# Optimization experiments

Measured on AMD Instinct MI355X. Metric: run time of the kernel, lower is better.

The kernel has to match this reference:

```python
import jax, jax.numpy as jnp
import numpy as np

N_NODES = 50000
N_EDGES = 800000
IN_F = 256
OUT_F = 64
HEADS = 4
NEG_SLOPE = 0.2


def setup_inputs() -> dict:
    key = jax.random.key(0)
    ks = jax.random.split(key, 6)
    x = jax.random.normal(ks[0], (N_NODES, IN_F), dtype=jnp.float32)
    edge_index = jax.random.randint(ks[1], (2, N_EDGES), 0, N_NODES, dtype=jnp.int32)
    edge_weight = jax.random.uniform(ks[2], (N_EDGES,), dtype=jnp.float32)
    # Xavier-uniform-ish scale for params
    gain = float(np.sqrt(2.0 / (1.0 + NEG_SLOPE ** 2)))
    w_bound = gain * np.sqrt(6.0 / (IN_F + OUT_F))
    a_bound = gain * np.sqrt(6.0 / (OUT_F + 1))
    W = jax.random.uniform(ks[3], (HEADS, IN_F, OUT_F), minval=-w_bound, maxval=w_bound, dtype=jnp.float32)
    a_src = jax.random.uniform(ks[4], (HEADS, OUT_F, 1), minval=-a_bound, maxval=a_bound, dtype=jnp.float32)
    a_dst = jax.random.uniform(ks[5], (HEADS, OUT_F, 1), minval=-a_bound, maxval=a_bound, dtype=jnp.float32)
    return {"x": x, "edge_index": edge_index, "edge_weight": edge_weight,
            "W": W, "a_src": a_src, "a_dst": a_dst}


def reference(x, edge_index, edge_weight, W, a_src, a_dst):
    num_nodes = x.shape[0]
    # Per-head linear projection: [H, N, out]
    h = jnp.einsum('ni,hio->hno', x, W)
    # Per-node attention logits, [H, N]
    attn_src = jnp.einsum('hno,hod->hn', h, a_src)
    attn_dst = jnp.einsum('hno,hod->hn', h, a_dst)
    src_idx, dst_idx = edge_index[0], edge_index[1]
    # Per-edge scores [H, E]
    e = attn_src[:, src_idx] + attn_dst[:, dst_idx]
    e = jnp.where(e >= 0, e, NEG_SLOPE * e)  # leaky_relu
    e = e * edge_weight[None, :]
    # Global-max-stabilized exp (matches original: single global max)
    e_exp = jnp.exp(e - jnp.max(e))
    # Segment-softmax denominator per dst node, [H, N]
    denom = jax.ops.segment_sum(e_exp.T, dst_idx, num_segments=num_nodes).T
    alpha = e_exp / (denom[:, dst_idx] + 1e-10)  # [H, E]
    # Weighted messages and scatter-add aggregation
    msg = h[:, src_idx] * alpha[..., None]  # [H, E, out]
    out = jax.vmap(lambda m: jax.ops.segment_sum(m, dst_idx, num_segments=num_nodes))(msg)  # [H, N, out]
    # concat=True: [N, H*out]
    return jnp.transpose(out, (1, 0, 2)).reshape(num_nodes, HEADS * OUT_F)
```

## Files before the change

### kernel.cpp

```cpp
#include <hip/hip_runtime.h>

#define N_NODES 50000
#define N_EDGES 800000
#define IN_F 256
#define OUT_F 64
#define HEADS 4
#define HF 256
#define NEG_SLOPE 0.2f

typedef __bf16 bf16x8 __attribute__((ext_vector_type(8)));
typedef float f32x4 __attribute__((ext_vector_type(4)));

__device__ __forceinline__ unsigned encf(float f) {
  unsigned u = __float_as_uint(f);
  return (u & 0x80000000u) ? ~u : (u | 0x80000000u);
}
__device__ __forceinline__ float decf(unsigned k) {
  unsigned u = (k & 0x80000000u) ? (k & 0x7FFFFFFFu) : ~k;
  return __uint_as_float(u);
}
__device__ __forceinline__ unsigned short f2bf(float f) {
  unsigned u = __float_as_uint(f);
  u += 0x7FFFu + ((u >> 16) & 1u);
  return (unsigned short)(u >> 16);
}
__device__ __forceinline__ float bflo(unsigned u) { return __uint_as_float(u << 16); }
__device__ __forceinline__ float bfhi(unsigned u) { return __uint_as_float(u & 0xFFFF0000u); }

__global__ __launch_bounds__(256) void k_prep(const float* __restrict__ x,
                                              const float* __restrict__ W,
                                              const int* __restrict__ dst,
                                              unsigned short* __restrict__ xb,
                                              unsigned short* __restrict__ wb,
                                              int* __restrict__ deg) {
  int tid = blockIdx.x * 256 + threadIdx.x;
  {
    const float* px = x + (size_t)tid * 8;
    float4 v0 = *(const float4*)px;
    float4 v1 = *(const float4*)(px + 4);
    uint4 o;
    o.x = (unsigned)f2bf(v0.x) | ((unsigned)f2bf(v0.y) << 16);
    o.y = (unsigned)f2bf(v0.z) | ((unsigned)f2bf(v0.w) << 16);
    o.z = (unsigned)f2bf(v1.x) | ((unsigned)f2bf(v1.y) << 16);
    o.w = (unsigned)f2bf(v1.z) | ((unsigned)f2bf(v1.w) << 16);
    *(uint4*)(xb + (size_t)tid * 8) = o;
  }
  if (tid < N_EDGES) atomicAdd(deg + dst[tid], 1);
  if (tid < 65536) {
    int j = tid & 7, l = (tid >> 3) & 63, kt = (tid >> 9) & 7;
    int w = (tid >> 12) & 3, hd = (tid >> 14) & 3;
    int k = kt * 32 + (l >> 4) * 8 + j;
    int o = w * 16 + (l & 15);
    wb[tid] = f2bf(W[((size_t)hd * IN_F + k) * OUT_F + o]);
  }
}

__global__ __launch_bounds__(256) void k_gemm(const unsigned short* __restrict__ xb,
                                              const unsigned short* __restrict__ wb,
                                              const float* __restrict__ a_src,
                                              const float* __restrict__ a_dst,
                                              unsigned short* __restrict__ hb,
                                              float* __restrict__ as_out,
                                              float* __restrict__ ad_out) {
  const int t = threadIdx.x;
  const int hd = t >> 6, l = t & 63;
  const int quad = l >> 4, col = l & 15;
  const int blk = blockIdx.x;
  f32x4 acc[4][4];
#pragma unroll
  for (int ms = 0; ms < 4; ms++)
#pragma unroll
    for (int nt = 0; nt < 4; nt++) acc[ms][nt] = (f32x4){0.f, 0.f, 0.f, 0.f};

  const unsigned short* ab[4];
#pragma unroll
  for (int ms = 0; ms < 4; ms++) {
    int mt = blk * 4 + ms;
    if (mt > 3124) mt = 3124;
    ab[ms] = xb + (size_t)(mt * 16 + col) * IN_F + quad * 8;
  }
  const unsigned short* wbase = wb + (size_t)hd * 16384 + l * 8;

  for (int kt = 0; kt < 8; kt++) {
    union { uint4 u; bf16x8 v; } b[4], a[4];
#pragma unroll
    for (int nt = 0; nt < 4; nt++)
      b[nt].u = *(const uint4*)(wbase + (nt * 8 + kt) * 512);
#pragma unroll
    for (int ms = 0; ms < 4; ms++)
      a[ms].u = *(const uint4*)(ab[ms] + kt * 32);
#pragma unroll
    for (int ms = 0; ms < 4; ms++)
#pragma unroll
      for (int nt = 0; nt < 4; nt++)
        acc[ms][nt] = __builtin_amdgcn_mfma_f32_16x16x32_bf16(a[ms].v, b[nt].v, acc[ms][nt], 0, 0, 0);
  }

  float avs[4], avd[4];
#pragma unroll
  for (int nt = 0; nt < 4; nt++) {
    avs[nt] = a_src[hd * OUT_F + nt * 16 + col];
    avd[nt] = a_dst[hd * OUT_F + nt * 16 + col];
  }
#pragma unroll
  for (int ms = 0; ms < 4; ms++) {
    int mbase = blk * 64 + ms * 16 + quad * 4;
#pragma unroll
    for (int r = 0; r < 4; r++) {
      int m = mbase + r;
      float ps = 0.f, pd = 0.f;
#pragma unroll
      for (int nt = 0; nt < 4; nt++) {
        float hv = acc[ms][nt][r];
        if (m < N_NODES)
          hb[(size_t)m * HF + hd * OUT_F + nt * 16 + col] = f2bf(hv);
        ps += hv * avs[nt];
        pd += hv * avd[nt];
      }
#pragma unroll
      for (int off = 8; off > 0; off >>= 1) {
        ps += __shfl_down(ps, off, 16);
        pd += __shfl_down(pd, off, 16);
      }
      if (col == 0 && m < N_NODES) {
        as_out[m * 4 + hd] = ps;
        ad_out[m * 4 + hd] = pd;
      }
    }
  }
}

__global__ __launch_bounds__(256) void k_alloc_scan(const int* __restrict__ deg,
                                                    int* __restrict__ alloc,
                                                    int* __restrict__ row_start,
                                                    int* __restrict__ cursor) {
  int i = blockIdx.x * 256 + threadIdx.x;
  int lane = threadIdx.x & 63, wv = threadIdx.x >> 6;
  int orig = (i < N_NODES) ? deg[i] : 0;
  int v = orig;
#pragma unroll
  for (int s = 1; s < 64; s <<= 1) {
    int u = __shfl_up(v, s);
    if (lane >= s) v += u;
  }
  __shared__ int wsum[4];
  __shared__ int sbase;
  if (lane == 63) wsum[wv] = v;
  __syncthreads();
  int base = 0;
  for (int w = 0; w < wv; w++) base += wsum[w];
  if (threadIdx.x == 0)
    sbase = atomicAdd(alloc, wsum[0] + wsum[1] + wsum[2] + wsum[3]);
  __syncthreads();
  if (i < N_NODES) {
    int rs = sbase + base + v - orig;
    row_start[i] = rs;
    cursor[i] = rs;
  }
}

__global__ __launch_bounds__(256) void k_scatter_max(const int* __restrict__ src,
                                                     const int* __restrict__ dst,
                                                     const float* __restrict__ ew,
                                                     const float* __restrict__ as,
                                                     const float* __restrict__ ad,
                                                     int* __restrict__ cursor,
                                                     int2* __restrict__ rec,
                                                     unsigned* __restrict__ gmax) {
  int t2 = blockIdx.x * 256 + threadIdx.x;
  bool ok = t2 * 2 < N_EDGES;
  int2 s2 = ok ? *(const int2*)(src + t2 * 2) : make_int2(0, 0);
  int2 d2 = ok ? *(const int2*)(dst + t2 * 2) : make_int2(0, 0);
  float2 w2 = ok ? *(const float2*)(ew + t2 * 2) : make_float2(0.f, 0.f);

  int pos0 = 0, pos1 = 0;
  if (ok) {
    pos0 = atomicAdd(cursor + d2.x, 1);
    pos1 = atomicAdd(cursor + d2.y, 1);
  }
  float4 a0, b0, a1, b1;
  if (ok) {
    a0 = *(const float4*)(as + (size_t)s2.x * 4);
    b0 = *(const float4*)(ad + (size_t)d2.x * 4);
    a1 = *(const float4*)(as + (size_t)s2.y * 4);
    b1 = *(const float4*)(ad + (size_t)d2.y * 4);
  } else {
    a0 = b0 = a1 = b1 = make_float4(0.f, 0.f, 0.f, 0.f);
  }
  if (ok) {
    rec[pos0] = make_int2(s2.x, __float_as_int(w2.x));
    rec[pos1] = make_int2(s2.y, __float_as_int(w2.y));
  }

  float m = -3.4e38f;
  if (ok) {
    float v0 = a0.x + b0.x, v1 = a0.y + b0.y, v2 = a0.z + b0.z, v3 = a0.w + b0.w;
    v0 = v0 >= 0.f ? v0 : NEG_SLOPE * v0;
    v1 = v1 >= 0.f ? v1 : NEG_SLOPE * v1;
    v2 = v2 >= 0.f ? v2 : NEG_SLOPE * v2;
    v3 = v3 >= 0.f ? v3 : NEG_SLOPE * v3;
    m = fmaxf(fmaxf(v0 * w2.x, v1 * w2.x), fmaxf(v2 * w2.x, v3 * w2.x));
    float u0 = a1.x + b1.x, u1 = a1.y + b1.y, u2 = a1.z + b1.z, u3 = a1.w + b1.w;
    u0 = u0 >= 0.f ? u0 : NEG_SLOPE * u0;
    u1 = u1 >= 0.f ? u1 : NEG_SLOPE * u1;
    u2 = u2 >= 0.f ? u2 : NEG_SLOPE * u2;
    u3 = u3 >= 0.f ? u3 : NEG_SLOPE * u3;
    m = fmaxf(m, fmaxf(fmaxf(u0 * w2.y, u1 * w2.y), fmaxf(u2 * w2.y, u3 * w2.y)));
  }
#pragma unroll
  for (int off = 32; off > 0; off >>= 1) m = fmaxf(m, __shfl_down(m, off));
  __shared__ float red[4];
  int wave = threadIdx.x >> 6, lane = threadIdx.x & 63;
  if (lane == 0) red[wave] = m;
  __syncthreads();
  if (threadIdx.x == 0) {
    float mm = fmaxf(fmaxf(red[0], red[1]), fmaxf(red[2], red[3]));
    atomicMax(gmax, encf(mm));
  }
}

__global__ __launch_bounds__(256) void k_agg(const int* __restrict__ row_start,
                                             const int* __restrict__ deg,
                                             const int2* __restrict__ rec,
                                             const float* __restrict__ as,
                                             const float* __restrict__ ad,
                                             const unsigned* __restrict__ gmax,
                                             const unsigned short* __restrict__ hb,
                                             float* __restrict__ out) {
  __shared__ float sal[4][4][68];
  const int t = threadIdx.x;
  const int wv = t >> 6, lane = t & 63;
  const int half = lane >> 5, li = lane & 31;
  const int hd8 = li >> 3;
  const int d = blockIdx.x * 4 + wv;
  const int rs = row_start[d];
  const int dg = deg[d];
  const float gm = decf(*gmax);
  const float4 adv = *(const float4*)(ad + (size_t)d * 4);
  float ax = 0.f, ay = 0.f, az = 0.f, aw = 0.f;
  float bx = 0.f, by = 0.f, bz = 0.f, bw = 0.f;
  float den = 0.f;

  for (int j0 = 0; j0 < dg; j0 += 64) {
    const int nj = min(64, dg - j0);
    int se = 0;
    float we = 0.f;
    if (lane < nj) {
      int2 r = rec[rs + j0 + lane];
      se = r.x;
      we = __int_as_float(r.y);
    }
    {
      float4 a4 = *(const float4*)(as + (size_t)se * 4);
      float v0 = a4.x + adv.x;
      float v1 = a4.y + adv.y;
      float v2 = a4.z + adv.z;
      float v3 = a4.w + adv.w;
      v0 = v0 >= 0.f ? v0 : NEG_SLOPE * v0;
      v1 = v1 >= 0.f ? v1 : NEG_SLOPE * v1;
      v2 = v2 >= 0.f ? v2 : NEG_SLOPE * v2;
      v3 = v3 >= 0.f ? v3 : NEG_SLOPE * v3;
      bool okj = lane < nj;
      sal[wv][0][lane] = okj ? __expf(v0 * we - gm) : 0.f;
      sal[wv][1][lane] = okj ? __expf(v1 * we - gm) : 0.f;
      sal[wv][2][lane] = okj ? __expf(v2 * we - gm) : 0.f;
      sal[wv][3][lane] = okj ? __expf(v3 * we - gm) : 0.f;
    }
    asm volatile("s_waitcnt lgkmcnt(0)" ::: "memory");
    const float* salh = sal[wv][hd8];

    int j = 0;
    for (; j + 7 < nj; j += 8) {
      int sj0 = __shfl(se, j + half);
      int sj1 = __shfl(se, j + 2 + half);
      int sj2 = __shfl(se, j + 4 + half);
      int sj3 = __shfl(se, j + 6 + half);
      uint4 q0 = *(const uint4*)(hb + (size_t)sj0 * HF + li * 8);
      uint4 q1 = *(const uint4*)(hb + (size_t)sj1 * HF + li * 8);
      uint4 q2 = *(const uint4*)(hb + (size_t)sj2 * HF + li * 8);
      uint4 q3 = *(const uint4*)(hb + (size_t)sj3 * HF + li * 8);
      float a0 = salh[j + half];
      float a1 = salh[j + 2 + half];
      float a2 = salh[j + 4 + half];
      float a3 = salh[j + 6 + half];
      den += (a0 + a1) + (a2 + a3);
      ax += a0 * bflo(q0.x) + a1 * bflo(q1.x) + a2 * bflo(q2.x) + a3 * bflo(q3.x);
      ay += a0 * bfhi(q0.x) + a1 * bfhi(q1.x) + a2 * bfhi(q2.x) + a3 * bfhi(q3.x);
      az += a0 * bflo(q0.y) + a1 * bflo(q1.y) + a2 * bflo(q2.y) + a3 * bflo(q3.y);
      aw += a0 * bfhi(q0.y) + a1 * bfhi(q1.y) + a2 * bfhi(q2.y) + a3 * bfhi(q3.y);
      bx += a0 * bflo(q0.z) + a1 * bflo(q1.z) + a2 * bflo(q2.z) + a3 * bflo(q3.z);
      by += a0 * bfhi(q0.z) + a1 * bfhi(q1.z) + a2 * bfhi(q2.z) + a3 * bfhi(q3.z);
      bz += a0 * bflo(q0.w) + a1 * bflo(q1.w) + a2 * bflo(q2.w) + a3 * bflo(q3.w);
      bw += a0 * bfhi(q0.w) + a1 * bfhi(q1.w) + a2 * bfhi(q2.w) + a3 * bfhi(q3.w);
    }
    for (; j < nj; j += 2) {
      int sj0 = __shfl(se, min(j + half, nj - 1));
      float a0 = (j + half < nj) ? salh[j + half] : 0.f;
      uint4 q0 = *(const uint4*)(hb + (size_t)sj0 * HF + li * 8);
      den += a0;
      ax += a0 * bflo(q0.x);
      ay += a0 * bfhi(q0.x);
      az += a0 * bflo(q0.y);
      aw += a0 * bfhi(q0.y);
      bx += a0 * bflo(q0.z);
      by += a0 * bfhi(q0.z);
      bz += a0 * bflo(q0.w);
      bw += a0 * bfhi(q0.w);
    }
  }

  ax += __shfl_xor(ax, 32); ay += __shfl_xor(ay, 32);
  az += __shfl_xor(az, 32); aw += __shfl_xor(aw, 32);
  bx += __shfl_xor(bx, 32); by += __shfl_xor(by, 32);
  bz += __shfl_xor(bz, 32); bw += __shfl_xor(bw, 32);
  den += __shfl_xor(den, 32);
  float inv = 1.f / (den + 1e-10f);
  float4 r;
  if (half == 0) r = make_float4(ax * inv, ay * inv, az * inv, aw * inv);
  else           r = make_float4(bx * inv, by * inv, bz * inv, bw * inv);
  *(float4*)(out + (size_t)d * HF + li * 8 + half * 4) = r;
}

extern "C" void kernel_launch(void* const* d_in, const int* in_sizes, int n_in,
                              void* d_out, int out_size, void* d_ws, size_t ws_size,
                              hipStream_t stream) {
  const float* x     = (const float*)d_in[0];
  const int*   ei    = (const int*)d_in[1];
  const float* ew    = (const float*)d_in[2];
  const float* W     = (const float*)d_in[3];
  const float* a_src = (const float*)d_in[4];
  const float* a_dst = (const float*)d_in[5];
  float* out = (float*)d_out;

  unsigned short* hb = (unsigned short*)d_ws;
  unsigned short* xb = hb + (size_t)N_NODES * HF;
  unsigned short* wbp = xb + (size_t)N_NODES * IN_F;
  float* as = (float*)(wbp + 65536);
  float* ad = as + (size_t)HEADS * N_NODES;
  int* deg       = (int*)(ad + (size_t)HEADS * N_NODES);
  int* alloc     = deg + N_NODES;
  unsigned* gmax = (unsigned*)(alloc + 1);
  int* row_start = (int*)(gmax + 1);
  int* cursor    = row_start + N_NODES;
  int2* rec      = (int2*)(cursor + N_NODES);

  const int* srcp = ei;
  const int* dstp = ei + N_EDGES;

  hipMemsetAsync(deg, 0, (size_t)(N_NODES + 2) * sizeof(int), stream);
  k_prep<<<6250, 256, 0, stream>>>(x, W, dstp, xb, wbp, deg);
  k_gemm<<<782, 256, 0, stream>>>(xb, wbp, a_src, a_dst, hb, as, ad);
  k_alloc_scan<<<(N_NODES + 255) / 256, 256, 0, stream>>>(deg, alloc, row_start, cursor);
  k_scatter_max<<<(N_EDGES / 2 + 255) / 256, 256, 0, stream>>>(srcp, dstp, ew, as, ad,
                                                               cursor, rec, gmax);
  k_agg<<<N_NODES / 4, 256, 0, stream>>>(row_start, deg, rec, as, ad, gmax, hb, out);
}
```

Before: 286.3 us.

## Precompute W·a vectors to get attention logits from x, fuse GEMM with edge scatter

Adds an init kernel that zeroes the counters and folds W with a_src/a_dst into per-head 256-length vectors. Attention logits are then computed directly from x in the prep kernel, so they no longer depend on the GEMM. This lets the bf16 MFMA GEMM and the edge scatter/max pass run as one launch with disjoint block ranges. It removes a memset, one kernel launch and the serialization between GEMM and scatter, at the cost of a small extra dot product per x chunk, with logits now taken from fp32 x instead of the bf16-rounded h.

```diff
diff --git a/kernel.cpp b/kernel.cpp
--- a/kernel.cpp
+++ b/kernel.cpp
@@ -27,17 +27,53 @@
 __device__ __forceinline__ float bflo(unsigned u) { return __uint_as_float(u << 16); }
 __device__ __forceinline__ float bfhi(unsigned u) { return __uint_as_float(u & 0xFFFF0000u); }
 
+__global__ __launch_bounds__(256) void k_init(const float* __restrict__ W,
+                                              const float* __restrict__ a_src,
+                                              const float* __restrict__ a_dst,
+                                              int* __restrict__ deg,
+                                              int* __restrict__ alloc,
+                                              unsigned* __restrict__ gmax,
+                                              float* __restrict__ wa_src,
+                                              float* __restrict__ wa_dst) {
+  if (blockIdx.x < 196) {
+    int i = blockIdx.x * 256 + threadIdx.x;
+    if (i < N_NODES) deg[i] = 0;
+    if (i == 0) { *alloc = 0; *gmax = 0u; }
+    return;
+  }
+  int hd = blockIdx.x - 196;
+  int k = threadIdx.x;
+  const float* wrow = W + ((size_t)hd * IN_F + k) * OUT_F;
+  const float* asv = a_src + hd * OUT_F;
+  const float* adv = a_dst + hd * OUT_F;
+  float ss = 0.f, sd = 0.f;
+#pragma unroll
+  for (int o = 0; o < OUT_F; o += 4) {
+    float4 w4 = *(const float4*)(wrow + o);
+    float4 s4 = *(const float4*)(asv + o);
+    float4 d4 = *(const float4*)(adv + o);
+    ss += w4.x * s4.x + w4.y * s4.y + w4.z * s4.z + w4.w * s4.w;
+    sd += w4.x * d4.x + w4.y * d4.y + w4.z * d4.z + w4.w * d4.w;
+  }
+  wa_src[hd * IN_F + k] = ss;
+  wa_dst[hd * IN_F + k] = sd;
+}
+
 __global__ __launch_bounds__(256) void k_prep(const float* __restrict__ x,
                                               const float* __restrict__ W,
                                               const int* __restrict__ dst,
+                                              const float* __restrict__ wa_src,
+                                              const float* __restrict__ wa_dst,
                                               unsigned short* __restrict__ xb,
                                               unsigned short* __restrict__ wb,
-                                              int* __restrict__ deg) {
+                                              int* __restrict__ deg,
+                                              float* __restrict__ as,
+                                              float* __restrict__ ad) {
   int tid = blockIdx.x * 256 + threadIdx.x;
+  const float* px = x + (size_t)tid * 8;
+  float4 v0 = *(const float4*)px;
+  float4 v1 = *(const float4*)(px + 4);
   {
-    const float* px = x + (size_t)tid * 8;
-    float4 v0 = *(const float4*)px;
-    float4 v1 = *(const float4*)(px + 4);
     uint4 o;
     o.x = (unsigned)f2bf(v0.x) | ((unsigned)f2bf(v0.y) << 16);
     o.y = (unsigned)f2bf(v0.z) | ((unsigned)f2bf(v0.w) << 16);
@@ -53,79 +89,32 @@
     int o = w * 16 + (l & 15);
     wb[tid] = f2bf(W[((size_t)hd * IN_F + k) * OUT_F + o]);
   }
-}
-
-__global__ __launch_bounds__(256) void k_gemm(const unsigned short* __restrict__ xb,
-                                              const unsigned short* __restrict__ wb,
-                                              const float* __restrict__ a_src,
-                                              const float* __restrict__ a_dst,
-                                              unsigned short* __restrict__ hb,
-                                              float* __restrict__ as_out,
-                                              float* __restrict__ ad_out) {
-  const int t = threadIdx.x;
-  const int hd = t >> 6, l = t & 63;
-  const int quad = l >> 4, col = l & 15;
-  const int blk = blockIdx.x;
-  f32x4 acc[4][4];
-#pragma unroll
-  for (int ms = 0; ms < 4; ms++)
-#pragma unroll
-    for (int nt = 0; nt < 4; nt++) acc[ms][nt] = (f32x4){0.f, 0.f, 0.f, 0.f};
-
-  const unsigned short* ab[4];
-#pragma unroll
-  for (int ms = 0; ms < 4; ms++) {
-    int mt = blk * 4 + ms;
-    if (mt > 3124) mt = 3124;
-    ab[ms] = xb + (size_t)(mt * 16 + col) * IN_F + quad * 8;
-  }
-  const unsigned short* wbase = wb + (size_t)hd * 16384 + l * 8;
-
-  for (int kt = 0; kt < 8; kt++) {
-    union { uint4 u; bf16x8 v; } b[4], a[4];
-#pragma unroll
-    for (int nt = 0; nt < 4; nt++)
-      b[nt].u = *(const uint4*)(wbase + (nt * 8 + kt) * 512);
-#pragma unroll
-    for (int ms = 0; ms < 4; ms++)
-      a[ms].u = *(const uint4*)(ab[ms] + kt * 32);
-#pragma unroll
-    for (int ms = 0; ms < 4; ms++)
-#pragma unroll
-      for (int nt = 0; nt < 4; nt++)
-        acc[ms][nt] = __builtin_amdgcn_mfma_f32_16x16x32_bf16(a[ms].v, b[nt].v, acc[ms][nt], 0, 0, 0);
-  }
-
-  float avs[4], avd[4];
-#pragma unroll
-  for (int nt = 0; nt < 4; nt++) {
-    avs[nt] = a_src[hd * OUT_F + nt * 16 + col];
-    avd[nt] = a_dst[hd * OUT_F + nt * 16 + col];
-  }
-#pragma unroll
-  for (int ms = 0; ms < 4; ms++) {
-    int mbase = blk * 64 + ms * 16 + quad * 4;
-#pragma unroll
-    for (int r = 0; r < 4; r++) {
-      int m = mbase + r;
-      float ps = 0.f, pd = 0.f;
-#pragma unroll
-      for (int nt = 0; nt < 4; nt++) {
-        float hv = acc[ms][nt][r];
-        if (m < N_NODES)
-          hb[(size_t)m * HF + hd * OUT_F + nt * 16 + col] = f2bf(hv);
-        ps += hv * avs[nt];
-        pd += hv * avd[nt];
+  {
+    int k0 = (tid & 31) * 8;
+    float ps[4], pd[4];
+#pragma unroll
+    for (int hd = 0; hd < 4; hd++) {
+      float4 s0 = *(const float4*)(wa_src + hd * IN_F + k0);
+      float4 s1 = *(const float4*)(wa_src + hd * IN_F + k0 + 4);
+      float4 d0 = *(const float4*)(wa_dst + hd * IN_F + k0);
+      float4 d1 = *(const float4*)(wa_dst + hd * IN_F + k0 + 4);
+      ps[hd] = v0.x * s0.x + v0.y * s0.y + v0.z * s0.z + v0.w * s0.w
+             + v1.x * s1.x + v1.y * s1.y + v1.z * s1.z + v1.w * s1.w;
+      pd[hd] = v0.x * d0.x + v0.y * d0.y + v0.z * d0.z + v0.w * d0.w
+             + v1.x * d1.x + v1.y * d1.y + v1.z * d1.z + v1.w * d1.w;
+    }
+#pragma unroll
+    for (int off = 16; off > 0; off >>= 1) {
+#pragma unroll
+      for (int hd = 0; hd < 4; hd++) {
+        ps[hd] += __shfl_down(ps[hd], off, 32);
+        pd[hd] += __shfl_down(pd[hd], off, 32);
       }
-#pragma unroll
-      for (int off = 8; off > 0; off >>= 1) {
-        ps += __shfl_down(ps, off, 16);
-        pd += __shfl_down(pd, off, 16);
-      }
-      if (col == 0 && m < N_NODES) {
-        as_out[m * 4 + hd] = ps;
-        ad_out[m * 4 + hd] = pd;
-      }
+    }
+    if ((tid & 31) == 0) {
+      int m = tid >> 5;
+      *(float4*)(as + (size_t)m * 4) = make_float4(ps[0], ps[1], ps[2], ps[3]);
+      *(float4*)(ad + (size_t)m * 4) = make_float4(pd[0], pd[1], pd[2], pd[3]);
     }
   }
 }
@@ -159,63 +148,112 @@
   }
 }
 
-__global__ __launch_bounds__(256) void k_scatter_max(const int* __restrict__ src,
-                                                     const int* __restrict__ dst,
-                                                     const float* __restrict__ ew,
-                                                     const float* __restrict__ as,
-                                                     const float* __restrict__ ad,
-                                                     int* __restrict__ cursor,
-                                                     int2* __restrict__ rec,
-                                                     unsigned* __restrict__ gmax) {
-  int t2 = blockIdx.x * 256 + threadIdx.x;
-  bool ok = t2 * 2 < N_EDGES;
-  int2 s2 = ok ? *(const int2*)(src + t2 * 2) : make_int2(0, 0);
-  int2 d2 = ok ? *(const int2*)(dst + t2 * 2) : make_int2(0, 0);
-  float2 w2 = ok ? *(const float2*)(ew + t2 * 2) : make_float2(0.f, 0.f);
-
-  int pos0 = 0, pos1 = 0;
-  if (ok) {
-    pos0 = atomicAdd(cursor + d2.x, 1);
-    pos1 = atomicAdd(cursor + d2.y, 1);
-  }
-  float4 a0, b0, a1, b1;
-  if (ok) {
-    a0 = *(const float4*)(as + (size_t)s2.x * 4);
-    b0 = *(const float4*)(ad + (size_t)d2.x * 4);
-    a1 = *(const float4*)(as + (size_t)s2.y * 4);
-    b1 = *(const float4*)(ad + (size_t)d2.y * 4);
-  } else {
-    a0 = b0 = a1 = b1 = make_float4(0.f, 0.f, 0.f, 0.f);
-  }
-  if (ok) {
-    rec[pos0] = make_int2(s2.x, __float_as_int(w2.x));
-    rec[pos1] = make_int2(s2.y, __float_as_int(w2.y));
-  }
-
-  float m = -3.4e38f;
-  if (ok) {
-    float v0 = a0.x + b0.x, v1 = a0.y + b0.y, v2 = a0.z + b0.z, v3 = a0.w + b0.w;
-    v0 = v0 >= 0.f ? v0 : NEG_SLOPE * v0;
-    v1 = v1 >= 0.f ? v1 : NEG_SLOPE * v1;
-    v2 = v2 >= 0.f ? v2 : NEG_SLOPE * v2;
-    v3 = v3 >= 0.f ? v3 : NEG_SLOPE * v3;
-    m = fmaxf(fmaxf(v0 * w2.x, v1 * w2.x), fmaxf(v2 * w2.x, v3 * w2.x));
-    float u0 = a1.x + b1.x, u1 = a1.y + b1.y, u2 = a1.z + b1.z, u3 = a1.w + b1.w;
-    u0 = u0 >= 0.f ? u0 : NEG_SLOPE * u0;
-    u1 = u1 >= 0.f ? u1 : NEG_SLOPE * u1;
-    u2 = u2 >= 0.f ? u2 : NEG_SLOPE * u2;
-    u3 = u3 >= 0.f ? u3 : NEG_SLOPE * u3;
-    m = fmaxf(m, fmaxf(fmaxf(u0 * w2.y, u1 * w2.y), fmaxf(u2 * w2.y, u3 * w2.y)));
-  }
-#pragma unroll
-  for (int off = 32; off > 0; off >>= 1) m = fmaxf(m, __shfl_down(m, off));
-  __shared__ float red[4];
-  int wave = threadIdx.x >> 6, lane = threadIdx.x & 63;
-  if (lane == 0) red[wave] = m;
-  __syncthreads();
-  if (threadIdx.x == 0) {
-    float mm = fmaxf(fmaxf(red[0], red[1]), fmaxf(red[2], red[3]));
-    atomicMax(gmax, encf(mm));
+__global__ __launch_bounds__(256) void k_gemm_scatter(
+    const unsigned short* __restrict__ xb, const unsigned short* __restrict__ wb,
+    unsigned short* __restrict__ hb,
+    const int* __restrict__ src, const int* __restrict__ dst,
+    const float* __restrict__ ew, const float* __restrict__ as,
+    const float* __restrict__ ad, int* __restrict__ cursor,
+    int2* __restrict__ rec, unsigned* __restrict__ gmax) {
+  const int t = threadIdx.x;
+
+  if (blockIdx.x >= 782) {
+    int t2 = (blockIdx.x - 782) * 256 + t;
+    bool ok = t2 * 2 < N_EDGES;
+    int2 s2 = ok ? *(const int2*)(src + t2 * 2) : make_int2(0, 0);
+    int2 d2 = ok ? *(const int2*)(dst + t2 * 2) : make_int2(0, 0);
+    float2 w2 = ok ? *(const float2*)(ew + t2 * 2) : make_float2(0.f, 0.f);
+    int pos0 = 0, pos1 = 0;
+    if (ok) {
+      pos0 = atomicAdd(cursor + d2.x, 1);
+      pos1 = atomicAdd(cursor + d2.y, 1);
+    }
+    float4 a0, b0, a1, b1;
+    if (ok) {
+      a0 = *(const float4*)(as + (size_t)s2.x * 4);
+      b0 = *(const float4*)(ad + (size_t)d2.x * 4);
+      a1 = *(const float4*)(as + (size_t)s2.y * 4);
+      b1 = *(const float4*)(ad + (size_t)d2.y * 4);
+    } else {
+      a0 = b0 = a1 = b1 = make_float4(0.f, 0.f, 0.f, 0.f);
+    }
+    if (ok) {
+      rec[pos0] = make_int2(s2.x, __float_as_int(w2.x));
+      rec[pos1] = make_int2(s2.y, __float_as_int(w2.y));
+    }
+    float m = -3.4e38f;
+    if (ok) {
+      float v0 = a0.x + b0.x, v1 = a0.y + b0.y, v2 = a0.z + b0.z, v3 = a0.w + b0.w;
+      v0 = v0 >= 0.f ? v0 : NEG_SLOPE * v0;
+      v1 = v1 >= 0.f ? v1 : NEG_SLOPE * v1;
+      v2 = v2 >= 0.f ? v2 : NEG_SLOPE * v2;
+      v3 = v3 >= 0.f ? v3 : NEG_SLOPE * v3;
+      m = fmaxf(fmaxf(v0 * w2.x, v1 * w2.x), fmaxf(v2 * w2.x, v3 * w2.x));
+      float u0 = a1.x + b1.x, u1 = a1.y + b1.y, u2 = a1.z + b1.z, u3 = a1.w + b1.w;
+      u0 = u0 >= 0.f ? u0 : NEG_SLOPE * u0;
+      u1 = u1 >= 0.f ? u1 : NEG_SLOPE * u1;
+      u2 = u2 >= 0.f ? u2 : NEG_SLOPE * u2;
+      u3 = u3 >= 0.f ? u3 : NEG_SLOPE * u3;
+      m = fmaxf(m, fmaxf(fmaxf(u0 * w2.y, u1 * w2.y), fmaxf(u2 * w2.y, u3 * w2.y)));
+    }
+#pragma unroll
+    for (int off = 32; off > 0; off >>= 1) m = fmaxf(m, __shfl_down(m, off));
+    __shared__ float red[4];
+    int wave = t >> 6, lane = t & 63;
+    if (lane == 0) red[wave] = m;
+    __syncthreads();
+    if (t == 0) {
+      float mm = fmaxf(fmaxf(red[0], red[1]), fmaxf(red[2], red[3]));
+      atomicMax(gmax, encf(mm));
+    }
+    return;
+  }
+
+  const int hd = t >> 6, l = t & 63;
+  const int quad = l >> 4, col = l & 15;
+  const int blk = blockIdx.x;
+  f32x4 acc[4][4];
+#pragma unroll
+  for (int ms = 0; ms < 4; ms++)
+#pragma unroll
+    for (int nt = 0; nt < 4; nt++) acc[ms][nt] = (f32x4){0.f, 0.f, 0.f, 0.f};
+
+  const unsigned short* ab[4];
+#pragma unroll
+  for (int ms = 0; ms < 4; ms++) {
+    int mt = blk * 4 + ms;
+    if (mt > 3124) mt = 3124;
+    ab[ms] = xb + (size_t)(mt * 16 + col) * IN_F + quad * 8;
+  }
+  const unsigned short* wbase = wb + (size_t)hd * 16384 + l * 8;
+
+  for (int kt = 0; kt < 8; kt++) {
+    union { uint4 u; bf16x8 v; } b[4], a[4];
+#pragma unroll
+    for (int nt = 0; nt < 4; nt++)
+      b[nt].u = *(const uint4*)(wbase + (nt * 8 + kt) * 512);
+#pragma unroll
+    for (int ms = 0; ms < 4; ms++)
+      a[ms].u = *(const uint4*)(ab[ms] + kt * 32);
+#pragma unroll
+    for (int ms = 0; ms < 4; ms++)
+#pragma unroll
+      for (int nt = 0; nt < 4; nt++)
+        acc[ms][nt] = __builtin_amdgcn_mfma_f32_16x16x32_bf16(a[ms].v, b[nt].v, acc[ms][nt], 0, 0, 0);
+  }
+
+#pragma unroll
+  for (int ms = 0; ms < 4; ms++) {
+    int mbase = blk * 64 + ms * 16 + quad * 4;
+#pragma unroll
+    for (int r = 0; r < 4; r++) {
+      int m = mbase + r;
+      if (m < N_NODES) {
+#pragma unroll
+        for (int nt = 0; nt < 4; nt++)
+          hb[(size_t)m * HF + hd * OUT_F + nt * 16 + col] = f2bf(acc[ms][nt][r]);
+      }
+    }
   }
 }
 
@@ -337,7 +375,9 @@
   unsigned short* wbp = xb + (size_t)N_NODES * IN_F;
   float* as = (float*)(wbp + 65536);
   float* ad = as + (size_t)HEADS * N_NODES;
-  int* deg       = (int*)(ad + (size_t)HEADS * N_NODES);
+  float* wa_src = ad + (size_t)HEADS * N_NODES;
+  float* wa_dst = wa_src + HEADS * IN_F;
+  int* deg       = (int*)(wa_dst + HEADS * IN_F);
   int* alloc     = deg + N_NODES;
   unsigned* gmax = (unsigned*)(alloc + 1);
   int* row_start = (int*)(gmax + 1);
@@ -347,11 +387,10 @@
   const int* srcp = ei;
   const int* dstp = ei + N_EDGES;
 
-  hipMemsetAsync(deg, 0, (size_t)(N_NODES + 2) * sizeof(int), stream);
-  k_prep<<<6250, 256, 0, stream>>>(x, W, dstp, xb, wbp, deg);
-  k_gemm<<<782, 256, 0, stream>>>(xb, wbp, a_src, a_dst, hb, as, ad);
-  k_alloc_scan<<<(N_NODES + 255) / 256, 256, 0, stream>>>(deg, alloc, row_start, cursor);
-  k_scatter_max<<<(N_EDGES / 2 + 255) / 256, 256, 0, stream>>>(srcp, dstp, ew, as, ad,
-                                                               cursor, rec, gmax);
+  k_init<<<200, 256, 0, stream>>>(W, a_src, a_dst, deg, alloc, gmax, wa_src, wa_dst);
+  k_prep<<<6250, 256, 0, stream>>>(x, W, dstp, wa_src, wa_dst, xb, wbp, deg, as, ad);
+  k_alloc_scan<<<196, 256, 0, stream>>>(deg, alloc, row_start, cursor);
+  k_gemm_scatter<<<2345, 256, 0, stream>>>(xb, wbp, hb, srcp, dstp, ew, as, ad,
+                                           cursor, rec, gmax);
   k_agg<<<N_NODES / 4, 256, 0, stream>>>(row_start, deg, rec, as, ad, gmax, hb, out);
 }
```

After: 272.0 us. -5.0%, faster.
